# Performance work log

Hardware: AMD Instinct MI355X
Metric: run time of the kernel (lower is better)

The kernel has to match this reference:

```python
import jax, jax.numpy as jnp
import numpy as np

NUM_HEADS = 16
HIDDEN = 1024
HEAD = HIDDEN // NUM_HEADS

def setup_inputs() -> dict:
    key = jax.random.key(0)
    k1, k2 = jax.random.split(key)
    embeddings = jax.random.normal(k1, (4, 2048, HIDDEN), dtype=jnp.float32)
    w_qkv = jax.random.normal(k2, (HIDDEN, 3 * HIDDEN), dtype=jnp.float32) * (1.0 / np.sqrt(HIDDEN))
    return {"embeddings": embeddings, "w_qkv": w_qkv}

def reference(embeddings, w_qkv):
    b, s, h = embeddings.shape
    # qkv projection (no bias): [b, s, 3*h]
    result = embeddings @ w_qkv
    # split '(qkv nah hdsz)': qkv outermost, then heads, then head dim
    result = result.reshape(b, s, 3, NUM_HEADS, HEAD)
    q = jnp.transpose(result[:, :, 0], (0, 2, 1, 3))  # [b, nah, s, hd]
    k = jnp.transpose(result[:, :, 1], (0, 2, 1, 3))
    v = jnp.transpose(result[:, :, 2], (0, 2, 1, 3))
    # NOTE: original scales by 1/sqrt(hidden_size), not 1/sqrt(head_size)
    scores = jnp.einsum('bnqd,bnkd->bnqk', q, k) / jnp.sqrt(jnp.float32(h))
    probs = jax.nn.softmax(scores, axis=-1)
    ctx = jnp.einsum('bnqk,bnkd->bnqd', probs, v)  # [b, nah, s, hd]
    out = jnp.transpose(ctx, (0, 2, 1, 3)).reshape(b, s, h)
    return out
```

## Files before the change

### kernel.cpp

```cpp
#include <hip/hip_runtime.h>
#include <hip/hip_bf16.h>


typedef __attribute__((ext_vector_type(8))) __bf16 bf16x8;
typedef __attribute__((ext_vector_type(8))) unsigned short u16x8;
typedef __attribute__((ext_vector_type(4))) unsigned short u16x4;
typedef __attribute__((ext_vector_type(4))) float f32x4;

#define B_  4
#define S_  2048
#define H_  1024
#define NH_ 16
#define HD_ 64
#define N3_ 3072
#define M_  (B_*S_)

static __device__ __forceinline__ unsigned short f2bf(float f) {
  __bf16 h = (__bf16)f;
  return __builtin_bit_cast(unsigned short, h);
}

static __device__ __forceinline__ float exp2_fast(float x) {
  float r; asm("v_exp_f32 %0, %1" : "=v"(r) : "v"(x)); return r;
}

static __device__ __forceinline__ void gload_lds16(const unsigned short* g,
                                                   unsigned short* l) {
  __builtin_amdgcn_global_load_lds(
      (const __attribute__((address_space(1))) unsigned int*)g,
      (__attribute__((address_space(3))) unsigned int*)l, 16, 0, 0);
}

__global__ __launch_bounds__(256) void cvt_emb_kernel(
    const float* __restrict__ in, unsigned short* __restrict__ out, int n4) {
  int i = blockIdx.x * blockDim.x + threadIdx.x;
  int stride = gridDim.x * blockDim.x;
  const float4* in4 = (const float4*)in;
  for (; i < n4; i += stride) {
    float4 v = in4[i];
    ushort4 o;
    o.x = f2bf(v.x); o.y = f2bf(v.y); o.z = f2bf(v.z); o.w = f2bf(v.w);
    ((ushort4*)out)[i] = o;
  }
}

__global__ __launch_bounds__(256) void cvt_w_kernel(
    const float* __restrict__ in, unsigned short* __restrict__ out) {
  __shared__ __align__(16) unsigned short tile[64 * 64];
  const int t = threadIdx.x;
  const int n0 = blockIdx.x * 64;
  const int k0 = blockIdx.y * 64;
#pragma unroll
  for (int it = 0; it < 4; ++it) {
    int c = it * 256 + t;
    int row = c >> 4;
    int a = c & 15;
    float4 v = *(const float4*)(in + (size_t)(k0 + row) * N3_ + n0 + a * 4);
    u16x4 o;
    o[0] = f2bf(v.x); o[1] = f2bf(v.y); o[2] = f2bf(v.z); o[3] = f2bf(v.w);
    int swz = (((row & 7) ^ ((row >> 3) & 7)) << 4);
    *(u16x4*)((char*)tile + row * 128 + ((a * 8) ^ swz)) = o;
  }
  __syncthreads();
#pragma unroll
  for (int it = 0; it < 2; ++it) {
    int c = it * 256 + t;
    int n = c >> 3;
    int a = c & 7;
    u16x8 o;
#pragma unroll
    for (int j = 0; j < 8; ++j) {
      int k = a * 8 + j;
      int swz = (((k & 7) ^ ((k >> 3) & 7)) << 4);
      o[j] = *(const unsigned short*)((char*)tile + k * 128 + ((2 * n) ^ swz));
    }
    *(u16x8*)(out + (size_t)(n0 + n) * H_ + k0 + a * 8) = o;
  }
}

__global__ __launch_bounds__(256, 3) void qkv_gemm_kernel(
    const unsigned short* __restrict__ A,
    const unsigned short* __restrict__ BT,
    unsigned short* __restrict__ C) {
  __shared__ __align__(16) unsigned short lds[2][2][128 * 32];
  const int t = threadIdx.x;
  const int lane = t & 63;
  const int w = t >> 6;
  const int wm = w >> 1, wn = w & 1;
  const int wg = blockIdx.x;
  const int swz = (wg & 7) * 192 + (wg >> 3);
  const int n0 = (swz % 24) * 128;
  const int m0 = (swz / 24) * 128;
  const int lr = lane & 15;
  const int lh = lane >> 4;
  const int ach = (lh ^ (lr & 3)) * 16;

  const int srow = w * 16 + (lane >> 2);
  const int sch = (lane & 3) ^ ((lane >> 2) & 3);
  const unsigned short* As = A + (size_t)(m0 + srow) * H_ + sch * 8;
  const unsigned short* Bs = BT + (size_t)(n0 + srow) * H_ + sch * 8;

#define STAGE(SB, KT)                                                        \
  do {                                                                       \
    gload_lds16(As + (size_t)(KT) * 32, &lds[SB][0][(w * 16) * 32]);         \
    gload_lds16(As + 64 * (size_t)H_ + (size_t)(KT) * 32,                    \
                &lds[SB][0][(64 + w * 16) * 32]);                            \
    gload_lds16(Bs + (size_t)(KT) * 32, &lds[SB][1][(w * 16) * 32]);         \
    gload_lds16(Bs + 64 * (size_t)H_ + (size_t)(KT) * 32,                    \
                &lds[SB][1][(64 + w * 16) * 32]);                            \
  } while (0)

  f32x4 acc[4][4];
#pragma unroll
  for (int i = 0; i < 4; i++)
#pragma unroll
    for (int j = 0; j < 4; j++)
#pragma unroll
      for (int r = 0; r < 4; r++) acc[i][j][r] = 0.f;

  STAGE(0, 0);
  __syncthreads();

  for (int kt = 0; kt < 32; ++kt) {
    const int cur = kt & 1;
    if (kt < 31) STAGE(cur ^ 1, kt + 1);
    bf16x8 af[4], bfr[4];
#pragma unroll
    for (int mi = 0; mi < 4; ++mi)
      af[mi] = *(const bf16x8*)((const char*)&lds[cur][0][0] +
                                (wm * 64 + mi * 16 + lr) * 64 + ach);
#pragma unroll
    for (int ni = 0; ni < 4; ++ni)
      bfr[ni] = *(const bf16x8*)((const char*)&lds[cur][1][0] +
                                 (wn * 64 + ni * 16 + lr) * 64 + ach);
#pragma unroll
    for (int mi = 0; mi < 4; ++mi)
#pragma unroll
      for (int ni = 0; ni < 4; ++ni)
        acc[mi][ni] = __builtin_amdgcn_mfma_f32_16x16x32_bf16(
            af[mi], bfr[ni], acc[mi][ni], 0, 0, 0);
    __syncthreads();
  }
#undef STAGE

  const float mult = (n0 < H_) ? 0.045084220027780106f : 1.0f;
#pragma unroll
  for (int mi = 0; mi < 4; mi++)
#pragma unroll
    for (int ni = 0; ni < 4; ni++)
#pragma unroll
      for (int rg = 0; rg < 4; rg++) {
        int row = m0 + wm * 64 + mi * 16 + lh * 4 + rg;
        int col = n0 + wn * 64 + ni * 16 + lr;
        C[(size_t)row * N3_ + col] = f2bf(acc[mi][ni][rg] * mult);
      }
}

__global__ __launch_bounds__(256) void vtrans_kernel(
    const unsigned short* __restrict__ qkv, unsigned short* __restrict__ vt) {
  __shared__ __align__(16) unsigned short tile[64 * 64];
  const int t = threadIdx.x;
  const int st = blockIdx.x;
  const int h = blockIdx.y;
  const int b = blockIdx.z;
  const int s0 = st * 64;
#pragma unroll
  for (int it = 0; it < 2; ++it) {
    int c = it * 256 + t;
    int row = c >> 3;
    int a = c & 7;
    u16x8 v = *(const u16x8*)(qkv + (size_t)(b * S_ + s0 + row) * N3_ +
                              2 * H_ + h * HD_ + a * 8);
    int swz = (((row & 7) ^ ((row >> 3) & 7)) << 4);
    *(u16x8*)((char*)tile + row * 128 + ((a * 16) ^ swz)) = v;
  }
  __syncthreads();
#pragma unroll
  for (int it = 0; it < 2; ++it) {
    int c = it * 256 + t;
    int d = c >> 3;
    int a = c & 7;
    u16x8 o;
#pragma unroll
    for (int j = 0; j < 8; ++j) {
      int r = a * 8 + j;
      int swz = (((r & 7) ^ ((r >> 3) & 7)) << 4);
      o[j] = *(const unsigned short*)((char*)tile + r * 128 + ((2 * d) ^ swz));
    }
    int s0a = a * 8, s0b = a * 8 + 4;
    int p_lo = ((s0a >> 5) << 3) | (((s0a >> 2) & 3) << 1) | ((s0a >> 4) & 1);
    int p_hi = ((s0b >> 5) << 3) | (((s0b >> 2) & 3) << 1) | ((s0b >> 4) & 1);
    unsigned short* dst =
        vt + ((size_t)((b * NH_ + h) * HD_) + d) * S_ + s0;
    u16x4 lo = {o[0], o[1], o[2], o[3]};
    u16x4 hi = {o[4], o[5], o[6], o[7]};
    *(u16x4*)(dst + p_lo * 4) = lo;
    *(u16x4*)(dst + p_hi * 4) = hi;
  }
}

__global__ __launch_bounds__(256, 3) void attn_kernel(
    const unsigned short* __restrict__ QKV,
    const unsigned short* __restrict__ VT,
    float* __restrict__ out) {
  __shared__ __align__(16) unsigned short k_lds[64 * 64];
  __shared__ __align__(16) unsigned short vt_lds[64 * 64];
  const int t = threadIdx.x;
  const int lane = t & 63;
  const int w = t >> 6;
  const int lr = lane & 15, lh = lane >> 4;
  const int h = blockIdx.y;
  const int b = blockIdx.z;
  const int qw = blockIdx.x * 128 + w * 32;

  bf16x8 qf[2][2];
#pragma unroll
  for (int qi = 0; qi < 2; ++qi) {
    const unsigned short* qp =
        QKV + (size_t)(b * S_ + qw + qi * 16 + lr) * N3_ + h * HD_ + lh * 8;
    qf[qi][0] = *(const bf16x8*)qp;
    qf[qi][1] = *(const bf16x8*)(qp + 32);
  }

  bf16x8 ones;
#pragma unroll
  for (int j = 0; j < 8; ++j) ones[j] = (lr == 0) ? (__bf16)1.0f : (__bf16)0.0f;

  f32x4 o[2][4], o5[2];
#pragma unroll
  for (int qi = 0; qi < 2; ++qi) {
#pragma unroll
    for (int i = 0; i < 4; i++)
#pragma unroll
      for (int r = 0; r < 4; r++) o[qi][i][r] = 0.f;
#pragma unroll
    for (int r = 0; r < 4; r++) o5[qi][r] = 0.f;
  }
  float mrun[2] = {-3e38f, -3e38f};

  const int row0 = t >> 3, a0 = t & 7;
  const int row1 = (256 + t) >> 3, a1 = t & 7;
  const int dst0 = row0 * 128 + ((a0 * 16) ^ ((row0 & 7) << 4));
  const int dst1 = row1 * 128 + ((a1 * 16) ^ ((row1 & 7) << 4));
  const unsigned short* kbase = QKV + (size_t)(b * S_) * N3_ + H_ + h * HD_;
  const unsigned short* vbase = VT + (size_t)((b * NH_ + h) * HD_) * S_;

  u16x8 gk0 = *(const u16x8*)(kbase + (size_t)row0 * N3_ + a0 * 8);
  u16x8 gk1 = *(const u16x8*)(kbase + (size_t)row1 * N3_ + a1 * 8);
  u16x8 gv0 = *(const u16x8*)(vbase + (size_t)row0 * S_ + a0 * 8);
  u16x8 gv1 = *(const u16x8*)(vbase + (size_t)row1 * S_ + a1 * 8);

  for (int kt = 0; kt < 32; ++kt) {
    __syncthreads();
    *(u16x8*)((char*)k_lds + dst0) = gk0;
    *(u16x8*)((char*)k_lds + dst1) = gk1;
    *(u16x8*)((char*)vt_lds + dst0) = gv0;
    *(u16x8*)((char*)vt_lds + dst1) = gv1;
    __syncthreads();

    {
      int ktn = (kt + 1) & 31;
      const unsigned short* kp = kbase + (size_t)(ktn * 64) * N3_;
      const unsigned short* vp = vbase + ktn * 64;
      gk0 = *(const u16x8*)(kp + (size_t)row0 * N3_ + a0 * 8);
      gk1 = *(const u16x8*)(kp + (size_t)row1 * N3_ + a1 * 8);
      gv0 = *(const u16x8*)(vp + (size_t)row0 * S_ + a0 * 8);
      gv1 = *(const u16x8*)(vp + (size_t)row1 * S_ + a1 * 8);
    }

    f32x4 sacc[2][4];
#pragma unroll
    for (int qi = 0; qi < 2; ++qi)
#pragma unroll
      for (int nt = 0; nt < 4; nt++)
#pragma unroll
        for (int r = 0; r < 4; r++) sacc[qi][nt][r] = 0.f;
#pragma unroll
    for (int nt = 0; nt < 4; ++nt) {
#pragma unroll
      for (int kb = 0; kb < 2; ++kb) {
        int row = nt * 16 + lr;
        bf16x8 kf = *(const bf16x8*)((char*)k_lds + row * 128 +
                                     ((64 * kb + 16 * lh) ^ ((row & 7) << 4)));
        sacc[0][nt] = __builtin_amdgcn_mfma_f32_16x16x32_bf16(kf, qf[0][kb], sacc[0][nt], 0, 0, 0);
        sacc[1][nt] = __builtin_amdgcn_mfma_f32_16x16x32_bf16(kf, qf[1][kb], sacc[1][nt], 0, 0, 0);
      }
    }

    float mx[2];
#pragma unroll
    for (int qi = 0; qi < 2; ++qi) {
      float m = fmaxf(fmaxf(fmaxf(sacc[qi][0][0], sacc[qi][0][1]),
                            fmaxf(sacc[qi][0][2], sacc[qi][0][3])),
                      fmaxf(fmaxf(sacc[qi][1][0], sacc[qi][1][1]),
                            fmaxf(sacc[qi][1][2], sacc[qi][1][3])));
      float m2 = fmaxf(fmaxf(fmaxf(sacc[qi][2][0], sacc[qi][2][1]),
                             fmaxf(sacc[qi][2][2], sacc[qi][2][3])),
                       fmaxf(fmaxf(sacc[qi][3][0], sacc[qi][3][1]),
                             fmaxf(sacc[qi][3][2], sacc[qi][3][3])));
      m = fmaxf(m, m2);
      m = fmaxf(m, __shfl_xor(m, 16, 64));
      m = fmaxf(m, __shfl_xor(m, 32, 64));
      mx[qi] = m;
    }

    bool ok = (mx[0] <= mrun[0] + 8.0f) && (mx[1] <= mrun[1] + 8.0f);
    if (!__all(ok)) {
#pragma unroll
      for (int qi = 0; qi < 2; ++qi) {
        float mn = fmaxf(mrun[qi], mx[qi]);
        float alpha = exp2_fast(mrun[qi] - mn);
        mrun[qi] = mn;
        float al[4];
#pragma unroll
        for (int rg = 0; rg < 4; ++rg) al[rg] = __shfl(alpha, lh * 4 + rg, 64);
#pragma unroll
        for (int dt = 0; dt < 4; ++dt)
#pragma unroll
          for (int rg = 0; rg < 4; ++rg) o[qi][dt][rg] *= al[rg];
#pragma unroll
        for (int rg = 0; rg < 4; ++rg) o5[qi][rg] *= al[rg];
      }
    }

    bf16x8 pa[2][2];
#pragma unroll
    for (int qi = 0; qi < 2; ++qi)
#pragma unroll
      for (int kb = 0; kb < 2; ++kb)
#pragma unroll
        for (int j = 0; j < 8; ++j)
          pa[qi][kb][j] =
              (__bf16)exp2_fast(sacc[qi][2 * kb + (j >> 2)][j & 3] - mrun[qi]);

#pragma unroll
    for (int kb = 0; kb < 2; ++kb) {
#pragma unroll
      for (int dt = 0; dt < 4; ++dt) {
        int row = dt * 16 + lr;
        bf16x8 vb = *(const bf16x8*)((char*)vt_lds + row * 128 +
                                     ((64 * kb + 16 * lh) ^ ((row & 7) << 4)));
        o[0][dt] = __builtin_amdgcn_mfma_f32_16x16x32_bf16(pa[0][kb], vb, o[0][dt], 0, 0, 0);
        o[1][dt] = __builtin_amdgcn_mfma_f32_16x16x32_bf16(pa[1][kb], vb, o[1][dt], 0, 0, 0);
      }
      o5[0] = __builtin_amdgcn_mfma_f32_16x16x32_bf16(pa[0][kb], ones, o5[0], 0, 0, 0);
      o5[1] = __builtin_amdgcn_mfma_f32_16x16x32_bf16(pa[1][kb], ones, o5[1], 0, 0, 0);
    }
  }

#pragma unroll
  for (int qi = 0; qi < 2; ++qi) {
    float inv[4];
#pragma unroll
    for (int rg = 0; rg < 4; ++rg) {
      float ls = __shfl(o5[qi][rg], lh * 16, 64);
      inv[rg] = 1.0f / ls;
    }
#pragma unroll
    for (int dt = 0; dt < 4; ++dt)
#pragma unroll
      for (int rg = 0; rg < 4; ++rg) {
        int qrow = qw + qi * 16 + lh * 4 + rg;
        out[(size_t)(b * S_ + qrow) * H_ + h * HD_ + dt * 16 + lr] =
            o[qi][dt][rg] * inv[rg];
      }
  }
}

extern "C" void kernel_launch(void* const* d_in, const int* in_sizes, int n_in,
                              void* d_out, int out_size, void* d_ws, size_t ws_size,
                              hipStream_t stream) {
  const float* emb = (const float*)d_in[0];
  const float* wqkv = (const float*)d_in[1];
  float* out = (float*)d_out;

  unsigned short* abf = (unsigned short*)d_ws;
  unsigned short* wtb = abf + (size_t)M_ * H_;
  unsigned short* qkv = wtb + (size_t)N3_ * H_;
  unsigned short* vt = abf;

  cvt_emb_kernel<<<dim3(2048), dim3(256), 0, stream>>>(emb, abf, (M_ * H_) / 4);
  cvt_w_kernel<<<dim3(48, 16), dim3(256), 0, stream>>>(wqkv, wtb);
  qkv_gemm_kernel<<<dim3(1536), dim3(256), 0, stream>>>(abf, wtb, qkv);
  vtrans_kernel<<<dim3(32, 16, 4), dim3(256), 0, stream>>>(qkv, vt);
  attn_kernel<<<dim3(16, 16, 4), dim3(256), 0, stream>>>(qkv, vt, out);
}
```

Baseline: 250.5 us.

## Triple-buffer QKV GEMM LDS pipeline with explicit vmcnt waits and setprio

```diff
diff --git a/kernel.cpp b/kernel.cpp
--- a/kernel.cpp
+++ b/kernel.cpp
@@ -78,11 +78,45 @@
   }
 }
 
+#define GEMM_ITER(BI, SB, KSTAGE, VM)                                        \
+  do {                                                                       \
+    asm volatile("s_waitcnt vmcnt(" VM ")" ::: "memory");                    \
+    __builtin_amdgcn_s_barrier();                                            \
+    __builtin_amdgcn_sched_barrier(0);                                       \
+    if ((KSTAGE) >= 0) {                                                     \
+      gload_lds16(As + (size_t)(KSTAGE) * 32, &lds[SB][0][(w * 16) * 32]);   \
+      gload_lds16(As + 64 * (size_t)H_ + (size_t)(KSTAGE) * 32,              \
+                  &lds[SB][0][(64 + w * 16) * 32]);                          \
+      gload_lds16(Bs + (size_t)(KSTAGE) * 32, &lds[SB][1][(w * 16) * 32]);   \
+      gload_lds16(Bs + 64 * (size_t)H_ + (size_t)(KSTAGE) * 32,              \
+                  &lds[SB][1][(64 + w * 16) * 32]);                          \
+    }                                                                        \
+    bf16x8 af[4], bfr[4];                                                    \
+    _Pragma("unroll")                                                        \
+    for (int mi = 0; mi < 4; ++mi)                                           \
+      af[mi] = *(const bf16x8*)((const char*)&lds[BI][0][0] +                \
+                                (wm * 64 + mi * 16 + lr) * 64 + ach);        \
+    _Pragma("unroll")                                                        \
+    for (int ni = 0; ni < 4; ++ni)                                           \
+      bfr[ni] = *(const bf16x8*)((const char*)&lds[BI][1][0] +               \
+                                 (wn * 64 + ni * 16 + lr) * 64 + ach);       \
+    asm volatile("s_waitcnt lgkmcnt(0)" ::: "memory");                       \
+    __builtin_amdgcn_sched_barrier(0);                                       \
+    __builtin_amdgcn_s_setprio(1);                                           \
+    _Pragma("unroll")                                                        \
+    for (int mi = 0; mi < 4; ++mi)                                           \
+      _Pragma("unroll")                                                      \
+      for (int ni = 0; ni < 4; ++ni)                                         \
+        acc[mi][ni] = __builtin_amdgcn_mfma_f32_16x16x32_bf16(               \
+            af[mi], bfr[ni], acc[mi][ni], 0, 0, 0);                          \
+    __builtin_amdgcn_s_setprio(0);                                           \
+  } while (0)
+
 __global__ __launch_bounds__(256, 3) void qkv_gemm_kernel(
     const unsigned short* __restrict__ A,
     const unsigned short* __restrict__ BT,
     unsigned short* __restrict__ C) {
-  __shared__ __align__(16) unsigned short lds[2][2][128 * 32];
+  __shared__ __align__(16) unsigned short lds[3][2][128 * 32];
   const int t = threadIdx.x;
   const int lane = t & 63;
   const int w = t >> 6;
@@ -100,16 +134,6 @@
   const unsigned short* As = A + (size_t)(m0 + srow) * H_ + sch * 8;
   const unsigned short* Bs = BT + (size_t)(n0 + srow) * H_ + sch * 8;
 
-#define STAGE(SB, KT)                                                        \
-  do {                                                                       \
-    gload_lds16(As + (size_t)(KT) * 32, &lds[SB][0][(w * 16) * 32]);         \
-    gload_lds16(As + 64 * (size_t)H_ + (size_t)(KT) * 32,                    \
-                &lds[SB][0][(64 + w * 16) * 32]);                            \
-    gload_lds16(Bs + (size_t)(KT) * 32, &lds[SB][1][(w * 16) * 32]);         \
-    gload_lds16(Bs + 64 * (size_t)H_ + (size_t)(KT) * 32,                    \
-                &lds[SB][1][(64 + w * 16) * 32]);                            \
-  } while (0)
-
   f32x4 acc[4][4];
 #pragma unroll
   for (int i = 0; i < 4; i++)
@@ -118,30 +142,23 @@
 #pragma unroll
       for (int r = 0; r < 4; r++) acc[i][j][r] = 0.f;
 
-  STAGE(0, 0);
-  __syncthreads();
-
-  for (int kt = 0; kt < 32; ++kt) {
-    const int cur = kt & 1;
-    if (kt < 31) STAGE(cur ^ 1, kt + 1);
-    bf16x8 af[4], bfr[4];
-#pragma unroll
-    for (int mi = 0; mi < 4; ++mi)
-      af[mi] = *(const bf16x8*)((const char*)&lds[cur][0][0] +
-                                (wm * 64 + mi * 16 + lr) * 64 + ach);
-#pragma unroll
-    for (int ni = 0; ni < 4; ++ni)
-      bfr[ni] = *(const bf16x8*)((const char*)&lds[cur][1][0] +
-                                 (wn * 64 + ni * 16 + lr) * 64 + ach);
-#pragma unroll
-    for (int mi = 0; mi < 4; ++mi)
-#pragma unroll
-      for (int ni = 0; ni < 4; ++ni)
-        acc[mi][ni] = __builtin_amdgcn_mfma_f32_16x16x32_bf16(
-            af[mi], bfr[ni], acc[mi][ni], 0, 0, 0);
-    __syncthreads();
-  }
-#undef STAGE
+  gload_lds16(As, &lds[0][0][(w * 16) * 32]);
+  gload_lds16(As + 64 * (size_t)H_, &lds[0][0][(64 + w * 16) * 32]);
+  gload_lds16(Bs, &lds[0][1][(w * 16) * 32]);
+  gload_lds16(Bs + 64 * (size_t)H_, &lds[0][1][(64 + w * 16) * 32]);
+  gload_lds16(As + 32, &lds[1][0][(w * 16) * 32]);
+  gload_lds16(As + 64 * (size_t)H_ + 32, &lds[1][0][(64 + w * 16) * 32]);
+  gload_lds16(Bs + 32, &lds[1][1][(w * 16) * 32]);
+  gload_lds16(Bs + 64 * (size_t)H_ + 32, &lds[1][1][(64 + w * 16) * 32]);
+
+  for (int kt = 0; kt < 30; kt += 3) {
+    GEMM_ITER(0, 2, kt + 2, "4");
+    GEMM_ITER(1, 0, kt + 3, "4");
+    GEMM_ITER(2, 1, kt + 4, "4");
+  }
+  GEMM_ITER(0, 0, -1, "4");
+  GEMM_ITER(1, 0, -1, "0");
+#undef GEMM_ITER
 
   const float mult = (n0 < H_) ? 0.045084220027780106f : 1.0f;
 #pragma unroll
```

Measured after the change: 253.6 us. No clear change (+1.2%).
